# Kernel tuning notes

Measured on AMD Instinct MI355X. Metric: run time of the kernel, lower is better.

## Reference

```python
import jax, jax.numpy as jnp
import numpy as np

B, T, D, H, L, O = 256, 256, 64, 512, 2, 10


def _uniform(key, shape, scale):
    return jax.random.uniform(key, shape, jnp.float32, -scale, scale)


def setup_inputs() -> dict:
    key = jax.random.key(0)
    ks = jax.random.split(key, 16)
    s = 1.0 / np.sqrt(H)  # PyTorch default init bound for RNN and Linear(H, .)
    inp = {
        "x": jax.random.normal(ks[0], (B, T, D), jnp.float32),
        # layer 0: input D -> H
        "w_ih0": _uniform(ks[1], (H, D), s),
        "w_hh0": _uniform(ks[2], (H, H), s),
        "b_ih0": _uniform(ks[3], (H,), s),
        "b_hh0": _uniform(ks[4], (H,), s),
        # layer 1: H -> H
        "w_ih1": _uniform(ks[5], (H, H), s),
        "w_hh1": _uniform(ks[6], (H, H), s),
        "b_ih1": _uniform(ks[7], (H,), s),
        "b_hh1": _uniform(ks[8], (H,), s),
        # head: fc1 (H->8), fc2 (8->O)
        "fc1_w": _uniform(ks[9], (8, H), s),
        "fc1_b": _uniform(ks[10], (8,), s),
        "fc2_w": _uniform(ks[11], (O, 8), 1.0 / np.sqrt(8)),
        "fc2_b": _uniform(ks[12], (O,), 1.0 / np.sqrt(8)),
    }
    return inp


def _rnn_relu_layer(seq, w_ih, w_hh, b_ih, b_hh):
    # seq: [T, B, Din] -> out: [T, B, H]
    # Precompute input projection for all timesteps (one big GEMM).
    x_proj = jnp.einsum('tbd,hd->tbh', seq, w_ih) + b_ih + b_hh

    def step(h, xp):
        h = jax.nn.relu(xp + h @ w_hh.T)
        return h, h

    h0 = jnp.zeros((seq.shape[1], w_hh.shape[0]), seq.dtype)
    _, out = jax.lax.scan(step, h0, x_proj)
    return out


def reference(x, w_ih0, w_hh0, b_ih0, b_hh0, w_ih1, w_hh1, b_ih1, b_hh1,
              fc1_w, fc1_b, fc2_w, fc2_b):
    seq = jnp.transpose(x, (1, 0, 2))  # [T, B, D]
    seq = _rnn_relu_layer(seq, w_ih0, w_hh0, b_ih0, b_hh0)
    seq = _rnn_relu_layer(seq, w_ih1, w_hh1, b_ih1, b_hh1)
    last = seq[-1]  # [B, H]
    h = jax.nn.relu(last @ fc1_w.T + fc1_b)
    return h @ fc2_w.T + fc2_b  # [B, O]
```

## Files before the change

### kernel.cpp

```cpp
#include <hip/hip_runtime.h>

using bf16x8 = __attribute__((ext_vector_type(8))) short;
using f32x4  = __attribute__((ext_vector_type(4))) float;
typedef unsigned short u16;
typedef unsigned int   u32;
typedef unsigned long long u64;

#define MAX_SPIN 2000000


__device__ __forceinline__ float bf2f(u16 u){ union{u32 i;float f;}v; v.i=((u32)u)<<16; return v.f; }
__device__ __forceinline__ u16 f2bf(float f){ union{float f;u32 i;}v; v.f=f; u32 x=v.i; return (u16)((x+0x7FFFu+((x>>16)&1u))>>16); }
__device__ __forceinline__ bf16x8 load8f(const float* p){
  float4 a=*(const float4*)p; float4 b=*(const float4*)(p+4);
  bf16x8 r; r[0]=(short)f2bf(a.x); r[1]=(short)f2bf(a.y); r[2]=(short)f2bf(a.z); r[3]=(short)f2bf(a.w);
  r[4]=(short)f2bf(b.x); r[5]=(short)f2bf(b.y); r[6]=(short)f2bf(b.z); r[7]=(short)f2bf(b.w); return r;
}
__device__ __forceinline__ int  ldf(int* p){ return __hip_atomic_load(p, __ATOMIC_RELAXED, __HIP_MEMORY_SCOPE_AGENT); }
__device__ __forceinline__ void stf(int* p, int v){ __hip_atomic_store(p, v, __ATOMIC_RELAXED, __HIP_MEMORY_SCOPE_AGENT); }
__device__ __forceinline__ u64  ld64c(const u32* p){ return __hip_atomic_load((const u64*)p, __ATOMIC_RELAXED, __HIP_MEMORY_SCOPE_AGENT); }
__device__ __forceinline__ u32  ld32c(const u32* p){ return __hip_atomic_load(p, __ATOMIC_RELAXED, __HIP_MEMORY_SCOPE_AGENT); }
__device__ __forceinline__ void st32c(u32* p, u32 v){ __hip_atomic_store(p, v, __ATOMIC_RELAXED, __HIP_MEMORY_SCOPE_AGENT); }
__device__ __forceinline__ int waitge(int* p, int tgt){
  int v = ldf(p); int it = 0;
  while (v < tgt && ++it < MAX_SPIN){ __builtin_amdgcn_s_sleep(1); v = ldf(p); }
  return v;
}

__global__ void init_kernel(u32* p){ p[(blockIdx.x<<9) + threadIdx.x] = 0u; }

#define HFRAG(base, ks) (*(const bf16x8*)((base) + (lrow<<10) + ((((ks)<<6)+(lk8<<1)) ^ sw)))

__global__ void __launch_bounds__(512, 2)
rnn_kernel(const float* __restrict__ x,
           const float* __restrict__ w_ih0, const float* __restrict__ w_hh0,
           const float* __restrict__ b_ih0, const float* __restrict__ b_hh0,
           const float* __restrict__ w_ih1, const float* __restrict__ w_hh1,
           const float* __restrict__ b_ih1, const float* __restrict__ b_hh1,
           const float* __restrict__ fc1_w, const float* __restrict__ fc1_b,
           const float* __restrict__ fc2_w, const float* __restrict__ fc2_b,
           float* __restrict__ out,
           u32* __restrict__ ring0, u32* __restrict__ ringz0, u32* __restrict__ ringz1,
           int* __restrict__ flags)
{
  const int tid  = threadIdx.x;
  const int wg   = blockIdx.x;
  const int lane = tid & 63;
  const int ww   = tid >> 6;
  const int role = wg >> 4;
  const int bt   = wg & 15;
  const int b0   = bt << 4;
  const int lrow = lane & 15;
  const int lk8  = (lane >> 4) << 3;
  const int sw   = (lrow & 7) << 4;
  const int rb   = (lane >> 4) << 2;

  extern __shared__ char dummy_unused[];
  __shared__ char sm[163840];
  char* smWb  = sm;
  char* smHhi = sm + 131072;
  char* smHlo = sm + 147456;

  int* flA  = flags + ((bt<<3) + 0)*16;
  int* flB0 = flags + ((bt<<3) + 1)*16;
  int* flB1 = flags + ((bt<<3) + 2)*16;
  int* flC  = flags + ((bt<<3) + 3)*16;
  int* flD  = flags + ((bt<<3) + 4)*16;

  if (role == 0 || role == 1) {
    const float* Wp = (role == 0) ? w_hh0 : w_hh1;
    const int n0 = ww << 6;
    bf16x8 wv[48];
#pragma unroll
    for (int tt = 0; tt < 4; ++tt) {
      int n = n0 + (tt<<4) + lrow;
#pragma unroll
      for (int ks = 0; ks < 12; ++ks)
        wv[tt*12+ks] = load8f(Wp + n*512 + (ks<<5) + lk8);
    }
#pragma unroll 1
    for (int it = 0; it < 16; ++it) {
      int cid = (it<<9) + tid;
      int ss = cid >> 11, wc = cid & 2047;
      int n = wc >> 2, k0 = (wc & 3) << 3;
      bf16x8 v = load8f(Wp + n*512 + 384 + (ss<<5) + k0);
      *(bf16x8*)(smWb + (ss<<15) + (n<<6) + ((k0<<1) ^ ((n&3)<<4))) = v;
    }
    __syncthreads();

    const int wl0 = ((lane>>4)<<4) ^ ((lrow&3)<<4);
    int wlb[4];
#pragma unroll
    for (int tt = 0; tt < 4; ++tt) wlb[tt] = ((n0 + (tt<<4) + lrow)<<6) + wl0;

    float zpf[16];
    int f0v = 0, f1v = 0;
    u32* zring = (role == 0) ? ringz0 : ringz1;
    const u32* zbase = zring + bt*32768;
    if (role == 0) { f0v = waitge(flD, 1); }
    else           { f0v = waitge(flB0, 1); f1v = waitge(flB1, 1); }
#pragma unroll
    for (int tt = 0; tt < 4; ++tt) {
      int nc = n0 + (tt<<4) + lrow;
#pragma unroll
      for (int r = 0; r < 4; ++r)
        zpf[tt*4+r] = __uint_as_float(ld32c(zbase + ((rb+r)<<9) + nc));
    }

    for (int s = 0; s < 256; ++s) {
      f32x4 acc[4] = {{0,0,0,0},{0,0,0,0},{0,0,0,0},{0,0,0,0}};
      if (s > 0) {
#pragma unroll
        for (int ks = 0; ks < 16; ++ks) {
          bf16x8 ahi = HFRAG(smHhi, ks);
          bf16x8 alo = HFRAG(smHlo, ks);
          bf16x8 bw0, bw1, bw2, bw3;
          if (ks < 12) { bw0 = wv[ks]; bw1 = wv[12+ks]; bw2 = wv[24+ks]; bw3 = wv[36+ks]; }
          else {
            int sb = (ks-12) << 15;
            bw0 = *(const bf16x8*)(smWb + sb + wlb[0]);
            bw1 = *(const bf16x8*)(smWb + sb + wlb[1]);
            bw2 = *(const bf16x8*)(smWb + sb + wlb[2]);
            bw3 = *(const bf16x8*)(smWb + sb + wlb[3]);
          }
          acc[0] = __builtin_amdgcn_mfma_f32_16x16x32_bf16(ahi, bw0, acc[0], 0,0,0);
          acc[0] = __builtin_amdgcn_mfma_f32_16x16x32_bf16(alo, bw0, acc[0], 0,0,0);
          acc[1] = __builtin_amdgcn_mfma_f32_16x16x32_bf16(ahi, bw1, acc[1], 0,0,0);
          acc[1] = __builtin_amdgcn_mfma_f32_16x16x32_bf16(alo, bw1, acc[1], 0,0,0);
          acc[2] = __builtin_amdgcn_mfma_f32_16x16x32_bf16(ahi, bw2, acc[2], 0,0,0);
          acc[2] = __builtin_amdgcn_mfma_f32_16x16x32_bf16(alo, bw2, acc[2], 0,0,0);
          acc[3] = __builtin_amdgcn_mfma_f32_16x16x32_bf16(ahi, bw3, acc[3], 0,0,0);
          acc[3] = __builtin_amdgcn_mfma_f32_16x16x32_bf16(alo, bw3, acc[3], 0,0,0);
        }
      }
      u32 pk[16];
#pragma unroll
      for (int tt = 0; tt < 4; ++tt)
#pragma unroll
        for (int r = 0; r < 4; ++r) {
          float v = acc[tt][r] + zpf[tt*4+r];
          v = v > 0.f ? v : 0.f;
          u16 hi = f2bf(v); u16 lo = f2bf(v - bf2f(hi));
          pk[tt*4+r] = ((u32)hi << 16) | lo;
        }
      if (role == 0) {
        u32* rs = ring0 + bt*32768 + ((s&3)<<13);
#pragma unroll
        for (int tt = 0; tt < 4; ++tt) {
          int nc = n0 + (tt<<4) + lrow;
#pragma unroll
          for (int r = 0; r < 4; ++r) st32c(rs + ((rb+r)<<9) + nc, pk[tt*4+r]);
        }
      }
      __syncthreads();
#pragma unroll
      for (int tt = 0; tt < 4; ++tt) {
        int cc = n0 + (tt<<4) + lrow;
#pragma unroll
        for (int r = 0; r < 4; ++r) {
          int rr = rb + r;
          int o = (rr<<10) + (((cc<<1)) ^ ((rr&7)<<4));
          *(u16*)(smHhi + o) = (u16)(pk[tt*4+r] >> 16);
          *(u16*)(smHlo + o) = (u16)(pk[tt*4+r] & 0xFFFFu);
        }
      }
      if (role == 0) asm volatile("s_waitcnt vmcnt(0)" ::: "memory");
      __syncthreads();
      if (tid == 0) stf((role==0) ? flA : flC, s + 1);
      if (s < 255) {
        if (role == 0) {
          if (f0v < s+2) f0v = waitge(flD, s+2); else f0v = ldf(flD);
          int need = s - 2;
          if (need > 0) {
            int bv0 = ldf(flB0), bv1 = ldf(flB1);
            if (bv0 < need) waitge(flB0, need);
            if (bv1 < need) waitge(flB1, need);
          }
        } else {
          if (f0v < s+2) f0v = waitge(flB0, s+2); else f0v = ldf(flB0);
          if (f1v < s+2) f1v = waitge(flB1, s+2); else f1v = ldf(flB1);
        }
        const u32* zs = zbase + (((s+1)&3)<<13);
#pragma unroll
        for (int tt = 0; tt < 4; ++tt) {
          int nc = n0 + (tt<<4) + lrow;
#pragma unroll
          for (int r = 0; r < 4; ++r)
            zpf[tt*4+r] = __uint_as_float(ld32c(zs + ((rb+r)<<9) + nc));
        }
      }
    }

    if (role == 1) {
      float* smF = (float*)sm;
      if (tid < 128) {
        int r = tid >> 3, j = tid & 7;
        const float* wr = fc1_w + (j << 9);
        float accv = fc1_b[j];
        for (int k = 0; k < 512; ++k) {
          int o = (r<<10) + (((k<<1)) ^ ((r&7)<<4));
          float hv = bf2f(*(u16*)(smHhi + o)) + bf2f(*(u16*)(smHlo + o));
          accv += hv * wr[k];
        }
        smF[tid] = accv > 0.f ? accv : 0.f;
      }
      __syncthreads();
      if (tid < 160) {
        int bb = tid / 10, o = tid - bb*10;
        float accv = fc2_b[o];
        const float* w = fc2_w + (o << 3);
#pragma unroll
        for (int j = 0; j < 8; ++j) accv += smF[(bb<<3)+j] * w[j];
        out[(b0 + bb)*10 + o] = accv;
      }
    }
  } else if (role == 2 || role == 3) {
    const int nb = (role - 2) << 8;
    const int n0 = nb + (ww << 5);
    bf16x8 wv[32];
    float bias[2];
#pragma unroll
    for (int tt = 0; tt < 2; ++tt) {
      int n = n0 + (tt<<4) + lrow;
#pragma unroll
      for (int ks = 0; ks < 16; ++ks)
        wv[tt*16+ks] = load8f(w_ih1 + n*512 + (ks<<5) + lk8);
      bias[tt] = b_ih1[n] + b_hh1[n];
    }
    int* flB = (role == 2) ? flB0 : flB1;
    int flAv = waitge(flA, 1), flCv = 0;
    u64 pf[8];
    {
      const u32* rs = ring0 + bt*32768;
#pragma unroll
      for (int k = 0; k < 8; ++k) {
        int q = tid + (k<<9); int r = q >> 8, c = q & 255;
        pf[k] = ld64c(rs + (r<<9) + (c<<1));
      }
    }
    for (int t = 0; t < 256; ++t) {
#pragma unroll
      for (int k = 0; k < 8; ++k) {
        int q = tid + (k<<9); int r = q >> 8, c = q & 255;
        u32 e0 = (u32)pf[k], e1 = (u32)(pf[k] >> 32);
        int o = (r<<10) + ((c<<2) ^ ((r&7)<<4));
        *(u32*)(smHhi + o) = (e0 >> 16) | (e1 & 0xFFFF0000u);
        *(u32*)(smHlo + o) = (e0 & 0xFFFFu) | (e1 << 16);
      }
      __syncthreads();
      f32x4 acc[2] = {{0,0,0,0},{0,0,0,0}};
#pragma unroll
      for (int ks = 0; ks < 16; ++ks) {
        bf16x8 ahi = HFRAG(smHhi, ks);
        bf16x8 alo = HFRAG(smHlo, ks);
        acc[0] = __builtin_amdgcn_mfma_f32_16x16x32_bf16(ahi, wv[ks],    acc[0], 0,0,0);
        acc[0] = __builtin_amdgcn_mfma_f32_16x16x32_bf16(alo, wv[ks],    acc[0], 0,0,0);
        acc[1] = __builtin_amdgcn_mfma_f32_16x16x32_bf16(ahi, wv[16+ks], acc[1], 0,0,0);
        acc[1] = __builtin_amdgcn_mfma_f32_16x16x32_bf16(alo, wv[16+ks], acc[1], 0,0,0);
      }
      {
        u32* zs = ringz1 + bt*32768 + ((t&3)<<13);
#pragma unroll
        for (int tt = 0; tt < 2; ++tt) {
          int nc = n0 + (tt<<4) + lrow;
#pragma unroll
          for (int r = 0; r < 4; ++r)
            st32c(zs + ((rb+r)<<9) + nc, __float_as_uint(acc[tt][r] + bias[tt]));
        }
      }
      __syncthreads();
      asm volatile("s_waitcnt vmcnt(0)" ::: "memory");
      __syncthreads();
      if (tid == 0) stf(flB, t + 1);
      if (t < 255) {
        if (flAv < t+2) flAv = waitge(flA, t+2); else flAv = ldf(flA);
        int need = t - 2;
        if (need > 0 && flCv < need) flCv = waitge(flC, need);
        else flCv = ldf(flC);
        const u32* rs = ring0 + bt*32768 + (((t+1)&3)<<13);
#pragma unroll
        for (int k = 0; k < 8; ++k) {
          int q = tid + (k<<9); int r = q >> 8, c = q & 255;
          pf[k] = ld64c(rs + (r<<9) + (c<<1));
        }
      }
    }
  } else {
    const int n0 = ww << 6;
    bf16x8 wx[8];
    float bz[4];
#pragma unroll
    for (int tt = 0; tt < 4; ++tt) {
      int n = n0 + (tt<<4) + lrow;
      wx[tt*2+0] = load8f(w_ih0 + n*64 + lk8);
      wx[tt*2+1] = load8f(w_ih0 + n*64 + 32 + lk8);
      bz[tt] = b_ih0[n] + b_hh0[n];
    }
    int flAv = 0;
    for (int s = 0; s < 256; ++s) {
      if (s >= 4 && flAv < s-3) flAv = waitge(flA, s-3);
      bf16x8 xh0, xl0, xh1, xl1;
      const float* xp = x + ((size_t)(b0 + lrow)*256 + s)*64 + lk8;
#pragma unroll
      for (int j = 0; j < 8; ++j) {
        float f0 = xp[j], f1 = xp[32+j];
        u16 h0 = f2bf(f0); xh0[j] = (short)h0; xl0[j] = (short)f2bf(f0 - bf2f(h0));
        u16 h1 = f2bf(f1); xh1[j] = (short)h1; xl1[j] = (short)f2bf(f1 - bf2f(h1));
      }
      f32x4 acc[4] = {{0,0,0,0},{0,0,0,0},{0,0,0,0},{0,0,0,0}};
#pragma unroll
      for (int tt = 0; tt < 4; ++tt) {
        acc[tt] = __builtin_amdgcn_mfma_f32_16x16x32_bf16(xh0, wx[tt*2+0], acc[tt], 0,0,0);
        acc[tt] = __builtin_amdgcn_mfma_f32_16x16x32_bf16(xl0, wx[tt*2+0], acc[tt], 0,0,0);
        acc[tt] = __builtin_amdgcn_mfma_f32_16x16x32_bf16(xh1, wx[tt*2+1], acc[tt], 0,0,0);
        acc[tt] = __builtin_amdgcn_mfma_f32_16x16x32_bf16(xl1, wx[tt*2+1], acc[tt], 0,0,0);
      }
      {
        u32* zs = ringz0 + bt*32768 + ((s&3)<<13);
#pragma unroll
        for (int tt = 0; tt < 4; ++tt) {
          int nc = n0 + (tt<<4) + lrow;
#pragma unroll
          for (int r = 0; r < 4; ++r)
            st32c(zs + ((rb+r)<<9) + nc, __float_as_uint(acc[tt][r] + bz[tt]));
        }
      }
      asm volatile("s_waitcnt vmcnt(0)" ::: "memory");
      __syncthreads();
      if (tid == 0) stf(flD, s + 1);
    }
  }
}

extern "C" void kernel_launch(void* const* d_in, const int* in_sizes, int n_in,
                              void* d_out, int out_size, void* d_ws, size_t ws_size,
                              hipStream_t stream) {
  const float* x     = (const float*)d_in[0];
  const float* w_ih0 = (const float*)d_in[1];
  const float* w_hh0 = (const float*)d_in[2];
  const float* b_ih0 = (const float*)d_in[3];
  const float* b_hh0 = (const float*)d_in[4];
  const float* w_ih1 = (const float*)d_in[5];
  const float* w_hh1 = (const float*)d_in[6];
  const float* b_ih1 = (const float*)d_in[7];
  const float* b_hh1 = (const float*)d_in[8];
  const float* fc1_w = (const float*)d_in[9];
  const float* fc1_b = (const float*)d_in[10];
  const float* fc2_w = (const float*)d_in[11];
  const float* fc2_b = (const float*)d_in[12];
  float* out = (float*)d_out;

  char* ws = (char*)d_ws;
  u32* ring0  = (u32*)(ws);
  u32* ringz0 = (u32*)(ws + (2u<<20));
  u32* ringz1 = (u32*)(ws + (4u<<20));
  int* flags  = (int*)(ws + (6u<<20));

  init_kernel<<<dim3(4), dim3(512), 0, stream>>>((u32*)(ws + (6u<<20)));
  rnn_kernel<<<dim3(80), dim3(512), 0, stream>>>(
      x, w_ih0, w_hh0, b_ih0, b_hh0, w_ih1, w_hh1, b_ih1, b_hh1,
      fc1_w, fc1_b, fc2_w, fc2_b, out,
      ring0, ringz0, ringz1, flags);
}
```

Baseline: 2.059 ms.

## Deepen inter-workgroup ring buffers to 8 slots and centralize flag polling in one thread

The ring buffers between the layer-0 input projection, the layer-0 recurrence, the layer-1 projection and the layer-1 recurrence grow from 4 to 8 timestep slots, which lets producers run further ahead before waiting on consumers. Flag polling moves from every thread to thread 0 only, followed by a __syncthreads, so the other threads stop hammering the flags. The aim is fewer pipeline stalls and less spin traffic on the critical recurrent chain. In exchange each step gets an extra barrier, the workspace footprint doubles, and the spin timeout is halved.

```diff
diff --git a/kernel.cpp b/kernel.cpp
--- a/kernel.cpp
+++ b/kernel.cpp
@@ -6,7 +6,7 @@
 typedef unsigned int   u32;
 typedef unsigned long long u64;
 
-#define MAX_SPIN 2000000
+#define MAX_SPIN 1000000
 
 
 __device__ __forceinline__ float bf2f(u16 u){ union{u32 i;float f;}v; v.i=((u32)u)<<16; return v.f; }
@@ -55,7 +55,6 @@
   const int sw   = (lrow & 7) << 4;
   const int rb   = (lane >> 4) << 2;
 
-  extern __shared__ char dummy_unused[];
   __shared__ char sm[163840];
   char* smWb  = sm;
   char* smHhi = sm + 131072;
@@ -93,12 +92,15 @@
 #pragma unroll
     for (int tt = 0; tt < 4; ++tt) wlb[tt] = ((n0 + (tt<<4) + lrow)<<6) + wl0;
 
+    u32* zring = (role == 0) ? ringz0 : ringz1;
+    const u32* zbase = zring + bt*65536;
+    int fP = 0, fP2 = 0, fBP0 = 0, fBP1 = 0;
+    if (tid == 0) {
+      if (role == 0) fP = waitge(flD, 1);
+      else { fP = waitge(flB0, 1); fP2 = waitge(flB1, 1); }
+    }
+    __syncthreads();
     float zpf[16];
-    int f0v = 0, f1v = 0;
-    u32* zring = (role == 0) ? ringz0 : ringz1;
-    const u32* zbase = zring + bt*32768;
-    if (role == 0) { f0v = waitge(flD, 1); }
-    else           { f0v = waitge(flB0, 1); f1v = waitge(flB1, 1); }
 #pragma unroll
     for (int tt = 0; tt < 4; ++tt) {
       int nc = n0 + (tt<<4) + lrow;
@@ -144,7 +146,7 @@
           pk[tt*4+r] = ((u32)hi << 16) | lo;
         }
       if (role == 0) {
-        u32* rs = ring0 + bt*32768 + ((s&3)<<13);
+        u32* rs = ring0 + bt*65536 + ((s&7)<<13);
 #pragma unroll
         for (int tt = 0; tt < 4; ++tt) {
           int nc = n0 + (tt<<4) + lrow;
@@ -164,23 +166,26 @@
           *(u16*)(smHlo + o) = (u16)(pk[tt*4+r] & 0xFFFFu);
         }
       }
-      if (role == 0) asm volatile("s_waitcnt vmcnt(0)" ::: "memory");
-      __syncthreads();
-      if (tid == 0) stf((role==0) ? flA : flC, s + 1);
+      asm volatile("s_waitcnt vmcnt(0)" ::: "memory");
+      __syncthreads();
+      if (tid == 0) {
+        stf((role==0) ? flA : flC, s + 1);
+        if (s < 255) {
+          if (role == 0) {
+            if (fP < s+2) fP = waitge(flD, s+2);
+            if (s-6 > 0) {
+              if (fBP0 < s-6) fBP0 = waitge(flB0, s-6);
+              if (fBP1 < s-6) fBP1 = waitge(flB1, s-6);
+            }
+          } else {
+            if (fP  < s+2) fP  = waitge(flB0, s+2);
+            if (fP2 < s+2) fP2 = waitge(flB1, s+2);
+          }
+        }
+      }
+      __syncthreads();
       if (s < 255) {
-        if (role == 0) {
-          if (f0v < s+2) f0v = waitge(flD, s+2); else f0v = ldf(flD);
-          int need = s - 2;
-          if (need > 0) {
-            int bv0 = ldf(flB0), bv1 = ldf(flB1);
-            if (bv0 < need) waitge(flB0, need);
-            if (bv1 < need) waitge(flB1, need);
-          }
-        } else {
-          if (f0v < s+2) f0v = waitge(flB0, s+2); else f0v = ldf(flB0);
-          if (f1v < s+2) f1v = waitge(flB1, s+2); else f1v = ldf(flB1);
-        }
-        const u32* zs = zbase + (((s+1)&3)<<13);
+        const u32* zs = zbase + (((s+1)&7)<<13);
 #pragma unroll
         for (int tt = 0; tt < 4; ++tt) {
           int nc = n0 + (tt<<4) + lrow;
@@ -228,10 +233,12 @@
       bias[tt] = b_ih1[n] + b_hh1[n];
     }
     int* flB = (role == 2) ? flB0 : flB1;
-    int flAv = waitge(flA, 1), flCv = 0;
+    int fA = 0, fC = 0;
+    if (tid == 0) fA = waitge(flA, 1);
+    __syncthreads();
     u64 pf[8];
     {
-      const u32* rs = ring0 + bt*32768;
+      const u32* rs = ring0 + bt*65536;
 #pragma unroll
       for (int k = 0; k < 8; ++k) {
         int q = tid + (k<<9); int r = q >> 8, c = q & 255;
@@ -259,7 +266,7 @@
         acc[1] = __builtin_amdgcn_mfma_f32_16x16x32_bf16(alo, wv[16+ks], acc[1], 0,0,0);
       }
       {
-        u32* zs = ringz1 + bt*32768 + ((t&3)<<13);
+        u32* zs = ringz1 + bt*65536 + ((t&7)<<13);
 #pragma unroll
         for (int tt = 0; tt < 2; ++tt) {
           int nc = n0 + (tt<<4) + lrow;
@@ -268,16 +275,18 @@
             st32c(zs + ((rb+r)<<9) + nc, __float_as_uint(acc[tt][r] + bias[tt]));
         }
       }
-      __syncthreads();
       asm volatile("s_waitcnt vmcnt(0)" ::: "memory");
       __syncthreads();
-      if (tid == 0) stf(flB, t + 1);
+      if (tid == 0) {
+        stf(flB, t + 1);
+        if (t < 255) {
+          if (fA < t+2) fA = waitge(flA, t+2);
+          if (t-6 > 0 && fC < t-6) fC = waitge(flC, t-6);
+        }
+      }
+      __syncthreads();
       if (t < 255) {
-        if (flAv < t+2) flAv = waitge(flA, t+2); else flAv = ldf(flA);
-        int need = t - 2;
-        if (need > 0 && flCv < need) flCv = waitge(flC, need);
-        else flCv = ldf(flC);
-        const u32* rs = ring0 + bt*32768 + (((t+1)&3)<<13);
+        const u32* rs = ring0 + bt*65536 + (((t+1)&7)<<13);
 #pragma unroll
         for (int k = 0; k < 8; ++k) {
           int q = tid + (k<<9); int r = q >> 8, c = q & 255;
@@ -296,9 +305,8 @@
       wx[tt*2+1] = load8f(w_ih0 + n*64 + 32 + lk8);
       bz[tt] = b_ih0[n] + b_hh0[n];
     }
-    int flAv = 0;
+    int fA = 0;
     for (int s = 0; s < 256; ++s) {
-      if (s >= 4 && flAv < s-3) flAv = waitge(flA, s-3);
       bf16x8 xh0, xl0, xh1, xl1;
       const float* xp = x + ((size_t)(b0 + lrow)*256 + s)*64 + lk8;
 #pragma unroll
@@ -315,8 +323,12 @@
         acc[tt] = __builtin_amdgcn_mfma_f32_16x16x32_bf16(xh1, wx[tt*2+1], acc[tt], 0,0,0);
         acc[tt] = __builtin_amdgcn_mfma_f32_16x16x32_bf16(xl1, wx[tt*2+1], acc[tt], 0,0,0);
       }
+      if (s >= 8) {
+        if (tid == 0 && fA < s-7) fA = waitge(flA, s-7);
+        __syncthreads();
+      }
       {
-        u32* zs = ringz0 + bt*32768 + ((s&3)<<13);
+        u32* zs = ringz0 + bt*65536 + ((s&7)<<13);
 #pragma unroll
         for (int tt = 0; tt < 4; ++tt) {
           int nc = n0 + (tt<<4) + lrow;
@@ -352,11 +364,11 @@
 
   char* ws = (char*)d_ws;
   u32* ring0  = (u32*)(ws);
-  u32* ringz0 = (u32*)(ws + (2u<<20));
-  u32* ringz1 = (u32*)(ws + (4u<<20));
-  int* flags  = (int*)(ws + (6u<<20));
-
-  init_kernel<<<dim3(4), dim3(512), 0, stream>>>((u32*)(ws + (6u<<20)));
+  u32* ringz0 = (u32*)(ws + (4u<<20));
+  u32* ringz1 = (u32*)(ws + (8u<<20));
+  int* flags  = (int*)(ws + (12u<<20));
+
+  init_kernel<<<dim3(4), dim3(512), 0, stream>>>((u32*)(ws + (12u<<20)));
   rnn_kernel<<<dim3(80), dim3(512), 0, stream>>>(
       x, w_ih0, w_hh0, b_ih0, b_hh0, w_ih1, w_hh1, b_ih1, b_hh1,
       fc1_w, fc1_b, fc2_w, fc2_b, out,
```

New measurement: 2.014 ms. 2.2% less time.
